# Performance work log

Measured on AMD Instinct MI355X. Metric: run time of the kernel, lower is better.

Reference implementation:

```python
import jax, jax.numpy as jnp
import numpy as np

B, NF, H = 1024, 64, 512


def setup_inputs() -> dict:
    key = jax.random.key(0)
    ks = jax.random.split(key, 12)
    sc_in2 = 1.0 / np.sqrt(2 * H)
    sc_in1 = 1.0 / np.sqrt(H)
    inp = {
        "field_vectors": jax.random.normal(ks[0], (B, NF, H), dtype=jnp.float32),
        # and_fusion: Linear(2H->H), ReLU, Linear(H->H)
        "and_W1": jax.random.uniform(ks[1], (2 * H, H), jnp.float32, -sc_in2, sc_in2),
        "and_b1": jax.random.uniform(ks[2], (H,), jnp.float32, -sc_in2, sc_in2),
        "and_W2": jax.random.uniform(ks[3], (H, H), jnp.float32, -sc_in1, sc_in1),
        "and_b2": jax.random.uniform(ks[4], (H,), jnp.float32, -sc_in1, sc_in1),
        # or_fusion: Linear(2H->H), ReLU, Linear(H->H)
        "or_W1": jax.random.uniform(ks[5], (2 * H, H), jnp.float32, -sc_in2, sc_in2),
        "or_b1": jax.random.uniform(ks[6], (H,), jnp.float32, -sc_in2, sc_in2),
        "or_W2": jax.random.uniform(ks[7], (H, H), jnp.float32, -sc_in1, sc_in1),
        "or_b2": jax.random.uniform(ks[8], (H,), jnp.float32, -sc_in1, sc_in1),
        # not_transform: Linear(H->H), Tanh
        "not_W": jax.random.uniform(ks[9], (H, H), jnp.float32, -sc_in1, sc_in1),
        "not_b": jax.random.uniform(ks[10], (H,), jnp.float32, -sc_in1, sc_in1),
        # Disjoint index structure so the torch skip-set logic is a no-op:
        # 'and' pairs use fields 0..31, 'or' pairs use 32..47, leftovers 48..63.
        "not_idx": 48 + jnp.arange(8, dtype=jnp.int32),
        "and_pairs": jnp.arange(32, dtype=jnp.int32).reshape(16, 2),
        "or_pairs": (32 + jnp.arange(16, dtype=jnp.int32)).reshape(8, 2),
        "leftover_idx": 48 + jnp.arange(16, dtype=jnp.int32),
    }
    return inp


def _mlp2(x, W1, b1, W2, b2):
    # Linear -> ReLU -> Linear
    return jax.nn.relu(x @ W1 + b1) @ W2 + b2


def reference(field_vectors, and_W1, and_b1, and_W2, and_b2,
              or_W1, or_b1, or_W2, or_b2, not_W, not_b,
              not_idx, and_pairs, or_pairs, leftover_idx):
    # In-place 'not' transform on selected fields (Tanh(Linear))
    fv = field_vectors.at[:, not_idx].set(
        jnp.tanh(field_vectors[:, not_idx] @ not_W + not_b))
    # Gather (i, j) pairs, concat along feature dim -> [B, P, 2H]
    cat_and = jnp.concatenate([fv[:, and_pairs[:, 0]], fv[:, and_pairs[:, 1]]], axis=-1)
    fused_and = _mlp2(cat_and, and_W1, and_b1, and_W2, and_b2)  # [B, 16, H]
    cat_or = jnp.concatenate([fv[:, or_pairs[:, 0]], fv[:, or_pairs[:, 1]]], axis=-1)
    fused_or = _mlp2(cat_or, or_W1, or_b1, or_W2, or_b2)  # [B, 8, H]
    # Stack order matches torch loop: and results, or results, untouched fields
    return jnp.concatenate([fused_and, fused_or, fv[:, leftover_idx]], axis=1)
```

## Files before the change

kernel.cpp:

```cpp
#include <hip/hip_runtime.h>
#include <hip/hip_bf16.h>
#include <math.h>

typedef __attribute__((ext_vector_type(8))) __bf16 bf16x8;
typedef __attribute__((ext_vector_type(4))) float f32x4;

__device__ __forceinline__ unsigned short f2bf(float f) {
    union { float f; unsigned u; } v; v.f = f;
    unsigned r = v.u + 0x7fffu + ((v.u >> 16) & 1u);
    return (unsigned short)(r >> 16);
}
__device__ __forceinline__ unsigned int pk(float a, float b) {
    union { float f; unsigned u; } x, y; x.f = a; y.f = b;
    unsigned ra = (x.u + 0x7fffu + ((x.u >> 16) & 1u)) >> 16;
    unsigned rb = (y.u + 0x7fffu + ((y.u >> 16) & 1u)) & 0xffff0000u;
    return ra | rb;
}

__device__ __forceinline__ void gl2lds16(const unsigned short* g, unsigned short* l) {
    __builtin_amdgcn_global_load_lds(
        (const __attribute__((address_space(1))) unsigned int*)(g),
        (__attribute__((address_space(3))) unsigned int*)(l), 16, 0, 0);
}

struct PrepArgs {
    const float* fv;
    unsigned short* fvb;
    const int* lidx;
    float* out;
    const float* W[5];
    unsigned short* WT[5];
    int K[5], N[5];
    int tstart[6];
};

__global__ __launch_bounds__(256) void prep_kernel(PrepArgs a) {
    __shared__ float tile[64][65];
    const int blk = blockIdx.x;
    const int tid = threadIdx.x;

    if (blk < 16384) {
        const int t = blk * 256 + tid;
        const float4* s = (const float4*)a.fv;
        const float4 v0 = s[2 * (size_t)t];
        const float4 v1 = s[2 * (size_t)t + 1];
        uint4 o;
        o.x = pk(v0.x, v0.y); o.y = pk(v0.z, v0.w);
        o.z = pk(v1.x, v1.y); o.w = pk(v1.z, v1.w);
        ((uint4*)a.fvb)[t] = o;
    } else if (blk < 24576) {
        const int t = (blk - 16384) * 256 + tid;
        const int c4 = t & 127, l = (t >> 7) & 15, b = t >> 11;
        const float4 v = *(const float4*)(a.fv + ((size_t)b * 64 + a.lidx[l]) * 512 + c4 * 4);
        *(float4*)(a.out + ((size_t)b * 40 + 24 + l) * 512 + c4 * 4) = v;
    } else {
        const int bx = blk - 24576;
        int m = 0;
        while (bx >= a.tstart[m + 1]) m++;
        const float* src = a.W[m];
        unsigned short* dst = a.WT[m];
        const int K = a.K[m], N = a.N[m];
        const int t = bx - a.tstart[m];
        const int ntn = N >> 6;
        const int tk = t / ntn, tn = t % ntn;
        const int c = tid & 63, r0 = tid >> 6;
        #pragma unroll
        for (int r = r0; r < 64; r += 4)
            tile[r][c] = src[(size_t)(tk * 64 + r) * N + tn * 64 + c];
        __syncthreads();
        #pragma unroll
        for (int r = r0; r < 64; r += 4)
            dst[(size_t)(tn * 64 + r) * K + tk * 64 + c] = f2bf(tile[c][r]);
    }
}

template <int P, int K, int SRCM, int EPIM, int QBASE>
__device__ __forceinline__ void gemm_seg(
    const unsigned short* __restrict__ A,
    const int* __restrict__ idx,
    const unsigned short* __restrict__ WT,
    const float* __restrict__ bias,
    unsigned short* __restrict__ hid_out,
    float* __restrict__ out,
    const int* __restrict__ leftover,
    int local,
    unsigned short* As, unsigned short* Bs) {

    const int tid  = threadIdx.x;
    const int lane = tid & 63, w = tid >> 6;
    const int tm = (local >> 2) * 128, tn = (local & 3) * 128;

    const int lm  = lane >> 2;
    const int kin = (lane & 3) * 8;
    const unsigned short* ar0[2];
    const unsigned short* ar1[2];
    const unsigned short* wp[2];
    #pragma unroll
    for (int c = 0; c < 2; c++) {
        const int m = tm + w * 32 + c * 16 + lm;
        if constexpr (SRCM == 0) {
            const int b = m / P, p = m % P;
            ar0[c] = A + ((size_t)b * 64 + idx[2 * p]) * 512;
            ar1[c] = A + ((size_t)b * 64 + idx[2 * p + 1]) * 512;
        } else if constexpr (SRCM == 1) {
            const int b = m >> 3, i = m & 7;
            ar0[c] = A + ((size_t)b * 64 + idx[i]) * 512;
        } else {
            ar0[c] = A + (size_t)m * K;
        }
        const int n = tn + w * 32 + c * 16 + lm;
        wp[c] = WT + (size_t)n * K;
    }

    f32x4 acc[4][4];
    #pragma unroll
    for (int i = 0; i < 4; i++)
        #pragma unroll
        for (int j = 0; j < 4; j++)
            acc[i][j] = f32x4{0.f, 0.f, 0.f, 0.f};

    const int wm = (w & 1) * 64, wn = (w >> 1) * 64;

    for (int k0 = 0; k0 < K; k0 += 32) {
        __syncthreads();
        #pragma unroll
        for (int c = 0; c < 2; c++) {
            const unsigned short* asrc;
            if constexpr (SRCM == 0)
                asrc = (k0 >= 512 ? ar1[c] + (k0 - 512) : ar0[c] + k0) + kin;
            else
                asrc = ar0[c] + k0 + kin;
            gl2lds16(asrc, &As[w * 1024 + c * 512]);
            gl2lds16(wp[c] + k0 + kin, &Bs[w * 1024 + c * 512]);
        }
        __syncthreads();

        bf16x8 af[4], bfr[4];
        #pragma unroll
        for (int mi = 0; mi < 4; mi++)
            af[mi] = *(const bf16x8*)&As[(wm + mi * 16 + (lane & 15)) * 32 + (lane >> 4) * 8];
        #pragma unroll
        for (int ni = 0; ni < 4; ni++)
            bfr[ni] = *(const bf16x8*)&Bs[(wn + ni * 16 + (lane & 15)) * 32 + (lane >> 4) * 8];
        #pragma unroll
        for (int mi = 0; mi < 4; mi++)
            #pragma unroll
            for (int ni = 0; ni < 4; ni++)
                acc[mi][ni] = __builtin_amdgcn_mfma_f32_16x16x32_bf16(
                    af[mi], bfr[ni], acc[mi][ni], 0, 0, 0);
    }

    const int col0 = tn + wn + (lane & 15);
    const int row0 = tm + wm + (lane >> 4) * 4;

    int qmap[8];
    if constexpr (EPIM == 2) {
        #pragma unroll
        for (int i = 0; i < 8; i++) {
            const int f = idx[i];
            int q = 24;
            for (int l = 0; l < 16; l++)
                if (leftover[l] == f) q = 24 + l;
            qmap[i] = q;
        }
    }

    #pragma unroll
    for (int ni = 0; ni < 4; ni++) {
        const int n  = col0 + ni * 16;
        const float bv = bias[n];
        #pragma unroll
        for (int mi = 0; mi < 4; mi++) {
            const int rbase = row0 + mi * 16;
            #pragma unroll
            for (int j = 0; j < 4; j++) {
                const int m = rbase + j;
                float v = acc[mi][ni][j] + bv;
                if constexpr (EPIM == 0) {
                    v = v > 0.f ? v : 0.f;
                    hid_out[(size_t)m * 512 + n] = f2bf(v);
                } else if constexpr (EPIM == 1) {
                    const int b = m / P, p = m % P;
                    out[((size_t)b * 40 + QBASE + p) * 512 + n] = v;
                } else {
                    const int b = m >> 3, i = m & 7;
                    out[((size_t)b * 40 + qmap[i]) * 512 + n] = tanhf(v);
                }
            }
        }
    }
}

struct L1Args {
    const unsigned short *fvb, *and_W1T, *or_W1T, *not_WT;
    const int *and_pairs, *or_pairs, *not_idx, *leftover;
    const float *and_b1, *or_b1, *not_b;
    unsigned short *and_hid, *or_hid;
    float* out;
};

__global__ __launch_bounds__(256, 3) void l1_phase(L1Args a) {
    __shared__ __align__(16) unsigned short As[128 * 32];
    __shared__ __align__(16) unsigned short Bs[128 * 32];
    const int blk = blockIdx.x;
    if (blk < 512)
        gemm_seg<16, 1024, 0, 0, 0>(a.fvb, a.and_pairs, a.and_W1T, a.and_b1,
                                    a.and_hid, nullptr, nullptr, blk, As, Bs);
    else if (blk < 768)
        gemm_seg<8, 1024, 0, 0, 0>(a.fvb, a.or_pairs, a.or_W1T, a.or_b1,
                                   a.or_hid, nullptr, nullptr, blk - 512, As, Bs);
    else
        gemm_seg<8, 512, 1, 2, 24>(a.fvb, a.not_idx, a.not_WT, a.not_b,
                                   nullptr, a.out, a.leftover, blk - 768, As, Bs);
}

struct L2Args {
    const unsigned short *and_hid, *or_hid, *and_W2T, *or_W2T;
    const float *and_b2, *or_b2;
    float* out;
};

__global__ __launch_bounds__(256, 3) void l2_phase(L2Args a) {
    __shared__ __align__(16) unsigned short As[128 * 32];
    __shared__ __align__(16) unsigned short Bs[128 * 32];
    const int blk = blockIdx.x;
    if (blk < 512)
        gemm_seg<16, 512, 2, 1, 0>(a.and_hid, nullptr, a.and_W2T, a.and_b2,
                                   nullptr, a.out, nullptr, blk, As, Bs);
    else
        gemm_seg<8, 512, 2, 1, 16>(a.or_hid, nullptr, a.or_W2T, a.or_b2,
                                   nullptr, a.out, nullptr, blk - 512, As, Bs);
}

extern "C" void kernel_launch(void* const* d_in, const int* in_sizes, int n_in,
                              void* d_out, int out_size, void* d_ws, size_t ws_size,
                              hipStream_t stream) {
    const float* fv       = (const float*)d_in[0];
    const float* and_W1   = (const float*)d_in[1];
    const float* and_b1   = (const float*)d_in[2];
    const float* and_W2   = (const float*)d_in[3];
    const float* and_b2   = (const float*)d_in[4];
    const float* or_W1    = (const float*)d_in[5];
    const float* or_b1    = (const float*)d_in[6];
    const float* or_W2    = (const float*)d_in[7];
    const float* or_b2    = (const float*)d_in[8];
    const float* not_W    = (const float*)d_in[9];
    const float* not_b    = (const float*)d_in[10];
    const int* not_idx    = (const int*)d_in[11];
    const int* and_pairs  = (const int*)d_in[12];
    const int* or_pairs   = (const int*)d_in[13];
    const int* leftover   = (const int*)d_in[14];
    float* out = (float*)d_out;
    char* ws = (char*)d_ws;

    unsigned short* fvb     = (unsigned short*)(ws);
    unsigned short* and_W1T = (unsigned short*)(ws + 67108864);
    unsigned short* or_W1T  = (unsigned short*)(ws + 68157440);
    unsigned short* and_W2T = (unsigned short*)(ws + 69206016);
    unsigned short* or_W2T  = (unsigned short*)(ws + 69730304);
    unsigned short* not_WT  = (unsigned short*)(ws + 70254592);
    unsigned short* and_hid = (unsigned short*)(ws + 70778880);
    unsigned short* or_hid  = (unsigned short*)(ws + 87556096);

    PrepArgs pa;
    pa.fv = fv; pa.fvb = fvb; pa.lidx = leftover; pa.out = out;
    pa.W[0] = and_W1; pa.WT[0] = and_W1T; pa.K[0] = 1024; pa.N[0] = 512;
    pa.W[1] = or_W1;  pa.WT[1] = or_W1T;  pa.K[1] = 1024; pa.N[1] = 512;
    pa.W[2] = and_W2; pa.WT[2] = and_W2T; pa.K[2] = 512;  pa.N[2] = 512;
    pa.W[3] = or_W2;  pa.WT[3] = or_W2T;  pa.K[3] = 512;  pa.N[3] = 512;
    pa.W[4] = not_W;  pa.WT[4] = not_WT;  pa.K[4] = 512;  pa.N[4] = 512;
    pa.tstart[0] = 0;   pa.tstart[1] = 128; pa.tstart[2] = 256;
    pa.tstart[3] = 320; pa.tstart[4] = 384; pa.tstart[5] = 448;
    prep_kernel<<<dim3(25024), dim3(256), 0, stream>>>(pa);

    L1Args g1;
    g1.fvb = fvb; g1.and_W1T = and_W1T; g1.or_W1T = or_W1T; g1.not_WT = not_WT;
    g1.and_pairs = and_pairs; g1.or_pairs = or_pairs; g1.not_idx = not_idx;
    g1.leftover = leftover;
    g1.and_b1 = and_b1; g1.or_b1 = or_b1; g1.not_b = not_b;
    g1.and_hid = and_hid; g1.or_hid = or_hid; g1.out = out;
    l1_phase<<<dim3(1024), dim3(256), 0, stream>>>(g1);

    L2Args g2;
    g2.and_hid = and_hid; g2.or_hid = or_hid;
    g2.and_W2T = and_W2T; g2.or_W2T = or_W2T;
    g2.and_b2 = and_b2; g2.or_b2 = or_b2; g2.out = out;
    l2_phase<<<dim3(768), dim3(256), 0, stream>>>(g2);
}
```

Baseline: 343.0 us.

## Fuse leftover copy into bf16 conversion, skip unused fields, swizzle LDS reads

The prep kernel now builds a per-field usage table in shared memory. It converts to bf16 only the fields that the and/or/not paths consume, and it copies leftover fields to the output from the same fp32 load, so the separate leftover-copy blocks go away. This removes one read of the leftover fields and skips loading fields that no later stage reads. It also applies an XOR swizzle to the column of the LDS tiles, both where the global-to-LDS copy writes and where the MFMA fragment loads read, to cut bank conflicts. The cost is a small per-block scan of the index arrays.

```diff
diff --git a/kernel.cpp b/kernel.cpp
--- a/kernel.cpp
+++ b/kernel.cpp
@@ -26,7 +26,7 @@
 struct PrepArgs {
     const float* fv;
     unsigned short* fvb;
-    const int* lidx;
+    const int *and_pairs, *or_pairs, *not_idx, *lidx;
     float* out;
     const float* W[5];
     unsigned short* WT[5];
@@ -36,25 +36,48 @@
 
 __global__ __launch_bounds__(256) void prep_kernel(PrepArgs a) {
     __shared__ float tile[64][65];
+    __shared__ int used[64];
+    __shared__ int lslot[64];
     const int blk = blockIdx.x;
     const int tid = threadIdx.x;
 
     if (blk < 16384) {
+        if (tid < 64) {
+            const int f = tid;
+            int u = 0;
+            for (int i = 0; i < 32; i++) u |= (a.and_pairs[i] == f);
+            for (int i = 0; i < 16; i++) u |= (a.or_pairs[i] == f);
+            for (int i = 0; i < 8; i++)  u |= (a.not_idx[i] == f);
+            used[f] = u;
+            int ls = -1;
+            for (int l = 0; l < 16; l++) if (a.lidx[l] == f) ls = l;
+            lslot[f] = ls;
+        }
+        __syncthreads();
+
         const int t = blk * 256 + tid;
-        const float4* s = (const float4*)a.fv;
-        const float4 v0 = s[2 * (size_t)t];
-        const float4 v1 = s[2 * (size_t)t + 1];
-        uint4 o;
-        o.x = pk(v0.x, v0.y); o.y = pk(v0.z, v0.w);
-        o.z = pk(v1.x, v1.y); o.w = pk(v1.z, v1.w);
-        ((uint4*)a.fvb)[t] = o;
-    } else if (blk < 24576) {
-        const int t = (blk - 16384) * 256 + tid;
-        const int c4 = t & 127, l = (t >> 7) & 15, b = t >> 11;
-        const float4 v = *(const float4*)(a.fv + ((size_t)b * 64 + a.lidx[l]) * 512 + c4 * 4);
-        *(float4*)(a.out + ((size_t)b * 40 + 24 + l) * 512 + c4 * 4) = v;
+        const size_t e = (size_t)t * 8;
+        const int c = (int)(e & 511);
+        const int f = (int)((e >> 9) & 63);
+        const int b = (int)(e >> 15);
+        const int u = used[f], ls = lslot[f];
+        if (u | (ls >= 0)) {
+            const float4 v0 = *(const float4*)(a.fv + e);
+            const float4 v1 = *(const float4*)(a.fv + e + 4);
+            if (u) {
+                uint4 o;
+                o.x = pk(v0.x, v0.y); o.y = pk(v0.z, v0.w);
+                o.z = pk(v1.x, v1.y); o.w = pk(v1.z, v1.w);
+                ((uint4*)a.fvb)[t] = o;
+            }
+            if (ls >= 0) {
+                float* d = a.out + ((size_t)b * 40 + 24 + ls) * 512 + c;
+                *(float4*)(d)     = v0;
+                *(float4*)(d + 4) = v1;
+            }
+        }
     } else {
-        const int bx = blk - 24576;
+        const int bx = blk - 16384;
         int m = 0;
         while (bx >= a.tstart[m + 1]) m++;
         const float* src = a.W[m];
@@ -91,7 +114,7 @@
     const int tm = (local >> 2) * 128, tn = (local & 3) * 128;
 
     const int lm  = lane >> 2;
-    const int kin = (lane & 3) * 8;
+    const int kin = (((lane & 3) ^ ((lane >> 2) & 3)) * 8);
     const unsigned short* ar0[2];
     const unsigned short* ar1[2];
     const unsigned short* wp[2];
@@ -120,6 +143,7 @@
             acc[i][j] = f32x4{0.f, 0.f, 0.f, 0.f};
 
     const int wm = (w & 1) * 64, wn = (w >> 1) * 64;
+    const int xsel = ((lane >> 4) ^ (lane & 3)) * 8;
 
     for (int k0 = 0; k0 < K; k0 += 32) {
         __syncthreads();
@@ -138,10 +162,10 @@
         bf16x8 af[4], bfr[4];
         #pragma unroll
         for (int mi = 0; mi < 4; mi++)
-            af[mi] = *(const bf16x8*)&As[(wm + mi * 16 + (lane & 15)) * 32 + (lane >> 4) * 8];
+            af[mi] = *(const bf16x8*)&As[(wm + mi * 16 + (lane & 15)) * 32 + xsel];
         #pragma unroll
         for (int ni = 0; ni < 4; ni++)
-            bfr[ni] = *(const bf16x8*)&Bs[(wn + ni * 16 + (lane & 15)) * 32 + (lane >> 4) * 8];
+            bfr[ni] = *(const bf16x8*)&Bs[(wn + ni * 16 + (lane & 15)) * 32 + xsel];
         #pragma unroll
         for (int mi = 0; mi < 4; mi++)
             #pragma unroll
@@ -263,7 +287,9 @@
     unsigned short* or_hid  = (unsigned short*)(ws + 87556096);
 
     PrepArgs pa;
-    pa.fv = fv; pa.fvb = fvb; pa.lidx = leftover; pa.out = out;
+    pa.fv = fv; pa.fvb = fvb; pa.out = out;
+    pa.and_pairs = and_pairs; pa.or_pairs = or_pairs;
+    pa.not_idx = not_idx; pa.lidx = leftover;
     pa.W[0] = and_W1; pa.WT[0] = and_W1T; pa.K[0] = 1024; pa.N[0] = 512;
     pa.W[1] = or_W1;  pa.WT[1] = or_W1T;  pa.K[1] = 1024; pa.N[1] = 512;
     pa.W[2] = and_W2; pa.WT[2] = and_W2T; pa.K[2] = 512;  pa.N[2] = 512;
@@ -271,7 +297,7 @@
     pa.W[4] = not_W;  pa.WT[4] = not_WT;  pa.K[4] = 512;  pa.N[4] = 512;
     pa.tstart[0] = 0;   pa.tstart[1] = 128; pa.tstart[2] = 256;
     pa.tstart[3] = 320; pa.tstart[4] = 384; pa.tstart[5] = 448;
-    prep_kernel<<<dim3(25024), dim3(256), 0, stream>>>(pa);
+    prep_kernel<<<dim3(16832), dim3(256), 0, stream>>>(pa);
 
     L1Args g1;
     g1.fvb = fvb; g1.and_W1T = and_W1T; g1.or_W1T = or_W1T; g1.not_WT = not_WT;
```

After: 342.6 us. About the same (-0.1%).
